# Kernel optimization log

Hardware: AMD Instinct MI355X
Metric: run time of the kernel (lower is better)

Reference implementation:

```python
import jax, jax.numpy as jnp
import numpy as np

B, S, HID = 2, 1024, 2048
N_HEADS, N_KV, HEAD_DIM = 32, 4, 128
BLOCK, MAX_BLOCKS = 32, 128
EPS = 1e-6
ROPE_THETA = 1e6


def _rmsnorm(x, w):
    # per-head RMSNorm over head_dim (Qwen3MoeRMSNorm)
    var = jnp.mean(x * x, axis=-1, keepdims=True)
    return x * jax.lax.rsqrt(var + EPS) * w


def _rotate_half(x):
    h = x.shape[-1] // 2
    return jnp.concatenate([-x[..., h:], x[..., :h]], axis=-1)


def setup_inputs() -> dict:
    key = jax.random.key(0)
    ks = jax.random.split(key, 8)
    hidden_states = jax.random.normal(ks[0], (B, S, HID), dtype=jnp.float32)
    wq = jax.random.normal(ks[1], (N_HEADS * HEAD_DIM, HID), dtype=jnp.float32) * 0.02
    wk = jax.random.normal(ks[2], (N_KV * HEAD_DIM, HID), dtype=jnp.float32) * 0.02
    wv = jax.random.normal(ks[3], (N_KV * HEAD_DIM, HID), dtype=jnp.float32) * 0.02
    wo = jax.random.normal(ks[4], (HID, N_HEADS * HEAD_DIM), dtype=jnp.float32) * 0.02
    q_norm_w = 1.0 + 0.01 * jax.random.normal(ks[5], (HEAD_DIM,), dtype=jnp.float32)
    k_norm_w = 1.0 + 0.01 * jax.random.normal(ks[6], (HEAD_DIM,), dtype=jnp.float32)
    # RoPE tables (rotate-half / llama convention)
    inv_freq = 1.0 / (ROPE_THETA ** (jnp.arange(0, HEAD_DIM, 2, dtype=jnp.float32) / HEAD_DIM))
    t = jnp.arange(S, dtype=jnp.float32)
    freqs = jnp.outer(t, inv_freq)  # [S, HEAD_DIM/2]
    emb = jnp.concatenate([freqs, freqs], axis=-1)  # [S, HEAD_DIM]
    cos, sin = jnp.cos(emb), jnp.sin(emb)
    # page table: B sequences x (S/BLOCK) blocks, distinct block ids
    page_table = jnp.arange(B * (S // BLOCK), dtype=jnp.int32).reshape(B, S // BLOCK)
    return {"hidden_states": hidden_states, "wq": wq, "wk": wk, "wv": wv, "wo": wo,
            "q_norm_w": q_norm_w, "k_norm_w": k_norm_w, "cos": cos, "sin": sin,
            "page_table": page_table}


def reference(hidden_states, wq, wk, wv, wo, q_norm_w, k_norm_w, cos, sin, page_table):
    b, s, _ = hidden_states.shape
    # fused QKV projection (math-equivalent to the concatenated qkv_proj_weight)
    q = (hidden_states @ wq.T).reshape(b, s, N_HEADS, HEAD_DIM)
    k = (hidden_states @ wk.T).reshape(b, s, N_KV, HEAD_DIM)
    v = (hidden_states @ wv.T).reshape(b, s, N_KV, HEAD_DIM)
    # per-head RMSNorm then RoPE
    q = _rmsnorm(q, q_norm_w)
    k = _rmsnorm(k, k_norm_w)
    c = cos[None, :, None, :]
    sn = sin[None, :, None, :]
    q = q * c + _rotate_half(q) * sn
    k = k * c + _rotate_half(k) * sn
    # paged KV-cache fill: [B, nblk, BLOCK, kvh, hd] -> cache[block_id, kvh, BLOCK, hd]
    nblk = s // BLOCK
    k_blk = k.reshape(b, nblk, BLOCK, N_KV, HEAD_DIM).transpose(0, 1, 3, 2, 4).reshape(-1, N_KV, BLOCK, HEAD_DIM)
    v_blk = v.reshape(b, nblk, BLOCK, N_KV, HEAD_DIM).transpose(0, 1, 3, 2, 4).reshape(-1, N_KV, BLOCK, HEAD_DIM)
    flat_pt = page_table.reshape(-1)
    cache_k = jnp.zeros((MAX_BLOCKS, N_KV, BLOCK, HEAD_DIM), dtype=k.dtype).at[flat_pt].set(k_blk)
    cache_v = jnp.zeros((MAX_BLOCKS, N_KV, BLOCK, HEAD_DIM), dtype=v.dtype).at[flat_pt].set(v_blk)
    # GQA: repeat kv heads (num_key_value_groups = 8)
    groups = N_HEADS // N_KV
    k_rep = jnp.repeat(k, groups, axis=2)  # [b, s, N_HEADS, hd]
    v_rep = jnp.repeat(v, groups, axis=2)
    # causal SDPA, scaling = head_dim ** -0.5
    scale = HEAD_DIM ** -0.5
    scores = jnp.einsum('bqhd,bkhd->bhqk', q, k_rep) * scale
    causal = jnp.tril(jnp.ones((s, s), dtype=bool))
    scores = jnp.where(causal[None, None], scores, jnp.finfo(scores.dtype).min)
    probs = jax.nn.softmax(scores, axis=-1)
    attn = jnp.einsum('bhqk,bkhd->bqhd', probs, v_rep).reshape(b, s, N_HEADS * HEAD_DIM)
    out = attn @ wo.T  # [b, s, HID]
    return out, cache_k, cache_v
```

## Files before the change

### kernel.cpp

```cpp
#include <hip/hip_runtime.h>
#include <hip/hip_bf16.h>


typedef __attribute__((ext_vector_type(8))) __bf16 bf16x8;
typedef __attribute__((ext_vector_type(4))) __bf16 bf16x4;
typedef __attribute__((ext_vector_type(4))) float f32x4;

__device__ __forceinline__ void gload16(const void* g, void* l) {
    __builtin_amdgcn_global_load_lds((const __attribute__((address_space(1))) void*)g,
                                     (__attribute__((address_space(3))) void*)l, 16, 0, 0);
}

__global__ __launch_bounds__(256) void cvt5(const float* __restrict__ s0, const float* __restrict__ s1,
                                            const float* __restrict__ s2, const float* __restrict__ s3,
                                            const float* __restrict__ s4,
                                            __bf16* __restrict__ d0, __bf16* __restrict__ d1,
                                            __bf16* __restrict__ d2, __bf16* __restrict__ d3,
                                            __bf16* __restrict__ d4) {
    const int b = blockIdx.x;
    const float* src; __bf16* dst; int off;
    if (b < 4096)       { src = s0; dst = d0; off = b; }
    else if (b < 12288) { src = s1; dst = d1; off = b - 4096; }
    else if (b < 13312) { src = s2; dst = d2; off = b - 12288; }
    else if (b < 14336) { src = s3; dst = d3; off = b - 13312; }
    else                { src = s4; dst = d4; off = b - 14336; }
    const int i = off * 256 + threadIdx.x;
    float4 v = reinterpret_cast<const float4*>(src)[i];
    bf16x4 o = {(__bf16)v.x, (__bf16)v.y, (__bf16)v.z, (__bf16)v.w};
    reinterpret_cast<bf16x4*>(dst)[i] = o;
}

__global__ __launch_bounds__(256) void reduce_add(float* __restrict__ o,
                                                  const float* __restrict__ p, int n4) {
    int i = blockIdx.x * 256 + threadIdx.x;
    int stride = gridDim.x * 256;
    for (; i < n4; i += stride) {
        float4 a = reinterpret_cast<float4*>(o)[i];
        float4 b = reinterpret_cast<const float4*>(p)[i];
        a.x += b.x; a.y += b.y; a.z += b.z; a.w += b.w;
        reinterpret_cast<float4*>(o)[i] = a;
    }
}

template <int NF, int OUT_BF16>
__global__ __launch_bounds__(512, 2) void gemm8p(const __bf16* __restrict__ A,
                                                 const __bf16* __restrict__ B,
                                                 void* __restrict__ C0,
                                                 void* __restrict__ C1,
                                                 const int M, const int N, const int K,
                                                 const int nTiles, const int nbn,
                                                 const int klen) {
    __shared__ __bf16 Asm[2 * 128 * 64];
    __shared__ __bf16 Bsm[2 * NF * 64 * 64];
    const int tid = threadIdx.x, lane = tid & 63, wave = tid >> 6;
    const int wm = wave >> 2, wn = wave & 3;
    const int lrow = lane & 15, lkg = lane >> 4;
    const int rsw = lrow & 7;
    const int bid = blockIdx.x;
    const int kz = bid / nTiles, tile = bid % nTiles;
    const int tswz = (tile & 7) * (nTiles >> 3) + (tile >> 3);
    const int bm = tswz / nbn, bn = tswz % nbn;
    const int brow = bm * 128, bcol = bn * (NF * 64);
    const int kbeg = kz * klen;
    const int row0 = tid >> 3;
    const int scol_sw = ((tid & 7) ^ (row0 & 7)) * 8;
    const __bf16* gA = A + (size_t)(brow + row0) * K + kbeg + scol_sw;
    const __bf16* gB = B + (size_t)(bcol + row0) * K + kbeg + scol_sw;
    const int slot0 = (lkg ^ rsw) * 8;
    const int slot1 = ((4 + lkg) ^ rsw) * 8;
    const int nt = klen / 64, nIter = nt / 2;

    f32x4 acc[4][NF] = {};
    bf16x8 areg[2], breg[NF];

    int su_t = 0, su_w = 0;
    auto stage1 = [&]() {
        if (su_t < nt) {
            const size_t ko = (size_t)su_t * 64;
            if (su_w < 2)
                gload16(gA + (size_t)(su_w * 64) * K + ko,
                        Asm + (su_t & 1) * 8192 + su_w * 4096 + tid * 8);
            else
                gload16(gB + (size_t)((su_w - 2) * 64) * K + ko,
                        Bsm + (su_t & 1) * (NF * 4096) + (su_w - 2) * 4096 + tid * 8);
        }
        if (++su_w == NF + 2) { su_w = 0; ++su_t; }
    };

    for (int u = 0; u < NF + 4; ++u) stage1();
    asm volatile("s_waitcnt vmcnt(2)" ::: "memory");
    __builtin_amdgcn_s_barrier();

    for (int i = 0; i < nIter; ++i) {
        const bool last = (i == nIter - 1);
#pragma unroll
        for (int p = 0; p < 8; ++p) {
            const int q = p & 3, kk = q >> 1, mfh = q & 1, cbuf = p >> 2;
            const __bf16* As = Asm + cbuf * 8192;
            const __bf16* Bs = Bsm + cbuf * (NF * 4096);
            const int ks = kk ? slot1 : slot0;
            if (mfh == 0) {
#pragma unroll
                for (int nf = 0; nf < NF; ++nf)
                    breg[nf] = *reinterpret_cast<const bf16x8*>(
                        &Bs[(wn * (NF * 16) + nf * 16 + lrow) * 64 + ks]);
            }
#pragma unroll
            for (int mi = 0; mi < 2; ++mi)
                areg[mi] = *reinterpret_cast<const bf16x8*>(
                    &As[(wm * 64 + (mfh * 2 + mi) * 16 + lrow) * 64 + ks]);
            const int cp = (NF == 5) ? ((q == 2) ? 1 : 2)
                                     : ((q == 1 || q == 2) ? 1 : 2);
            stage1();
            if (cp == 2) stage1();
            if (p == 3) {
                if (last) asm volatile("s_waitcnt vmcnt(0)" ::: "memory");
                else      asm volatile("s_waitcnt vmcnt(2)" ::: "memory");
            } else if (p == 7 && !last) {
                asm volatile("s_waitcnt vmcnt(2)" ::: "memory");
            }
            __builtin_amdgcn_s_barrier();
            asm volatile("s_waitcnt lgkmcnt(0)" ::: "memory");
            __builtin_amdgcn_sched_barrier(0);
            __builtin_amdgcn_s_setprio(1);
#pragma unroll
            for (int mi = 0; mi < 2; ++mi)
#pragma unroll
                for (int nf = 0; nf < NF; ++nf)
                    acc[mfh * 2 + mi][nf] = __builtin_amdgcn_mfma_f32_16x16x32_bf16(
                        areg[mi], breg[nf], acc[mfh * 2 + mi][nf], 0, 0, 0);
            __builtin_amdgcn_s_setprio(0);
            __builtin_amdgcn_s_barrier();
        }
    }

    void* C = (kz == 0) ? C0 : C1;
#pragma unroll
    for (int mi = 0; mi < 4; ++mi)
#pragma unroll
        for (int nf = 0; nf < NF; ++nf)
#pragma unroll
            for (int j = 0; j < 4; ++j) {
                const size_t r = brow + wm * 64 + mi * 16 + lkg * 4 + j;
                const size_t c = bcol + wn * (NF * 16) + nf * 16 + lrow;
                if (OUT_BF16)
                    ((__bf16*)C)[r * N + c] = (__bf16)acc[mi][nf][j];
                else
                    ((float*)C)[r * N + c] = acc[mi][nf][j];
            }
}

__global__ __launch_bounds__(256) void norm_rope_cache(
    __bf16* __restrict__ qkv, const float* __restrict__ cosT, const float* __restrict__ sinT,
    const float* __restrict__ qw, const float* __restrict__ kw,
    const int* __restrict__ ptab, float* __restrict__ cacheK, float* __restrict__ cacheV) {
    const int t = blockIdx.x;
    const int b = t >> 10, s = t & 1023;
    const int wave = threadIdx.x >> 6, lane = threadIdx.x & 63;
    __bf16* row = qkv + (size_t)t * 5120;
    const float c = cosT[s * 128 + lane];
    const float sn = sinT[s * 128 + lane];
    const int page = ptab[b * 32 + (s >> 5)];
    const int so = s & 31;
    const float wq0 = qw[lane], wq1 = qw[lane + 64];
#pragma unroll
    for (int i = 0; i < 8; ++i) {
        const int h = wave * 8 + i;
        float x0 = (float)row[h * 128 + lane];
        float x1 = (float)row[h * 128 + 64 + lane];
        float ss = x0 * x0 + x1 * x1;
        for (int off = 32; off; off >>= 1) ss += __shfl_xor(ss, off);
        const float rs = rsqrtf(ss * (1.0f / 128.0f) + 1e-6f);
        const float y0 = x0 * rs * wq0, y1 = x1 * rs * wq1;
        row[h * 128 + lane]      = (__bf16)(y0 * c - y1 * sn);
        row[h * 128 + 64 + lane] = (__bf16)(y1 * c + y0 * sn);
    }
    {
        const int h = wave;
        float x0 = (float)row[4096 + h * 128 + lane];
        float x1 = (float)row[4096 + h * 128 + 64 + lane];
        float ss = x0 * x0 + x1 * x1;
        for (int off = 32; off; off >>= 1) ss += __shfl_xor(ss, off);
        const float rs = rsqrtf(ss * (1.0f / 128.0f) + 1e-6f);
        const float y0 = x0 * rs * kw[lane], y1 = x1 * rs * kw[lane + 64];
        const float o0 = y0 * c - y1 * sn, o1 = y1 * c + y0 * sn;
        row[4096 + h * 128 + lane]      = (__bf16)o0;
        row[4096 + h * 128 + 64 + lane] = (__bf16)o1;
        float* ck = cacheK + (((size_t)page * 4 + h) * 32 + so) * 128;
        ck[lane] = o0; ck[lane + 64] = o1;
        const float v0 = (float)row[4608 + h * 128 + lane];
        const float v1 = (float)row[4608 + h * 128 + 64 + lane];
        float* cv = cacheV + (((size_t)page * 4 + h) * 32 + so) * 128;
        cv[lane] = v0; cv[lane + 64] = v1;
    }
}

__global__ __launch_bounds__(512, 2) void attn_fwd(const __bf16* __restrict__ qkv,
                                                   __bf16* __restrict__ out) {
    __shared__ __bf16 Ks[2][64 * 128];
    __shared__ __bf16 Vs[2][128 * 64];
    __shared__ __bf16 Ps[8][2][16 * 64];
    const int qa = blockIdx.x;
    const int qbig = 63 - qa;
    const int kvg = blockIdx.y, b = blockIdx.z;
    const int tid = threadIdx.x, wave = tid >> 6, lane = tid & 63;
    const int lrow = lane & 15, lkg = lane >> 4;
    const int h = kvg * 8 + wave;
    const size_t base = (size_t)b * 1024 * 5120;
    const int kofs = 4096 + kvg * 128, vofs = 4608 + kvg * 128;
    const int ntA = qa / 4 + 1, nt = qbig / 4 + 1;
    const int qposA = qa * 16 + lrow, qposB = qbig * 16 + lrow;
    const int rsw = lrow & 7;

    bf16x8 aqA[4], aqB[4];
#pragma unroll
    for (int kc = 0; kc < 4; ++kc) {
        bf16x8 ta = *reinterpret_cast<const bf16x8*>(
            &qkv[base + (size_t)(qa * 16 + lrow) * 5120 + h * 128 + kc * 32 + lkg * 8]);
        bf16x8 tb = *reinterpret_cast<const bf16x8*>(
            &qkv[base + (size_t)(qbig * 16 + lrow) * 5120 + h * 128 + kc * 32 + lkg * 8]);
#pragma unroll
        for (int i = 0; i < 8; ++i) {
            ta[i] = (__bf16)((float)ta[i] * 0.08838834764831845f);
            tb[i] = (__bf16)((float)tb[i] * 0.08838834764831845f);
        }
        aqA[kc] = ta; aqB[kc] = tb;
    }

    f32x4 accA[8] = {}, accB[8] = {};
    float mA = -1e30f, lA = 0.f, mB = -1e30f, lB = 0.f;
    __bf16* PwA = &Ps[wave][0][0];
    __bf16* PwB = &Ps[wave][1][0];

    auto stageK = [&](int t, int buf) {
        const int kv0 = (t < nt) ? t * 64 : 0;
#pragma unroll
        for (int c = 0; c < 2; ++c) {
            const int chunk = c * 8 + wave;
            const int row = chunk * 4 + (lane >> 4);
            const int gslot = (lane & 15) ^ (row & 7);
            gload16(&qkv[base + (size_t)(kv0 + row) * 5120 + kofs + gslot * 8],
                    &Ks[buf][chunk * 512]);
        }
    };
    auto loadV = [&](int t, uint4 (&vr)[2]) {
        const int kv0 = (t < nt) ? t * 64 : 0;
#pragma unroll
        for (int r = 0; r < 2; ++r)
            vr[r] = *reinterpret_cast<const uint4*>(
                &qkv[base + (size_t)(kv0 + lane) * 5120 + vofs + wave * 16 + r * 8]);
    };
    auto writeV = [&](uint4 (&vr)[2], int buf) {
#pragma unroll
        for (int r = 0; r < 2; ++r) {
            const __bf16* pv = reinterpret_cast<const __bf16*>(&vr[r]);
#pragma unroll
            for (int j = 0; j < 8; ++j) {
                const int d = wave * 16 + r * 8 + j;
                Vs[buf][d * 64 + (((lane >> 3) ^ j) << 3) + (lane & 7)] = pv[j];
            }
        }
    };

    auto smax = [&](f32x4 (&st)[4], float& m_i, float& l_i, f32x4 (&acc)[8],
                    int qpos, int kv0, bool maskit, __bf16* Pw) {
        float sv[16]; float pmax = -1e30f;
#pragma unroll
        for (int f = 0; f < 4; ++f)
#pragma unroll
            for (int j = 0; j < 4; ++j) {
                float x = st[f][j];
                if (maskit) {
                    const int kvpos = kv0 + f * 16 + lkg * 4 + j;
                    if (kvpos > qpos) x = -1e30f;
                }
                sv[f * 4 + j] = x;
                pmax = fmaxf(pmax, x);
            }
        pmax = fmaxf(pmax, __shfl_xor(pmax, 16));
        pmax = fmaxf(pmax, __shfl_xor(pmax, 32));
        if (!__all(pmax - m_i <= 8.f)) {
            const float m_new = fmaxf(m_i, pmax);
            const float sf = __expf(m_i - m_new);
            m_i = m_new;
            l_i *= sf;
            float sfj[4];
#pragma unroll
            for (int j = 0; j < 4; ++j) sfj[j] = __shfl(sf, lkg * 4 + j);
#pragma unroll
            for (int f = 0; f < 8; ++f)
#pragma unroll
                for (int j = 0; j < 4; ++j) acc[f][j] *= sfj[j];
        }
        float ladd = 0.f;
#pragma unroll
        for (int f = 0; f < 4; ++f) {
            bf16x4 pb;
#pragma unroll
            for (int j = 0; j < 4; ++j) {
                const float p = __expf(sv[f * 4 + j] - m_i);
                ladd += p;
                pb[j] = (__bf16)p;
            }
            const int slot = (f * 2 + (lkg >> 1)) ^ rsw;
            *reinterpret_cast<bf16x4*>(&Pw[lrow * 64 + slot * 8 + (lkg & 1) * 4]) = pb;
        }
        ladd += __shfl_xor(ladd, 16);
        ladd += __shfl_xor(ladd, 32);
        l_i += ladd;
    };

    auto body = [&](int t, uint4 (&vcur)[2], uint4 (&vnext)[2]) {
        const int kbuf = t & 1;
        __builtin_amdgcn_s_barrier();
        asm volatile("" ::: "memory");
        loadV(t + 1, vnext);
        stageK(t + 1, kbuf ^ 1);
        asm volatile("s_waitcnt vmcnt(4)" ::: "memory");
        writeV(vcur, kbuf);
        asm volatile("s_waitcnt lgkmcnt(0)" ::: "memory");
        __builtin_amdgcn_s_barrier();
        asm volatile("" ::: "memory");

        const bool doA = t < ntA;
        f32x4 stA[4] = {}, stB[4] = {};
#pragma unroll
        for (int kc = 0; kc < 4; ++kc)
#pragma unroll
            for (int f = 0; f < 4; ++f) {
                bf16x8 ak = *reinterpret_cast<const bf16x8*>(
                    &Ks[kbuf][(f * 16 + lrow) * 128 + (((kc * 4 + lkg) ^ rsw) << 3)]);
                stB[f] = __builtin_amdgcn_mfma_f32_16x16x32_bf16(ak, aqB[kc], stB[f], 0, 0, 0);
                if (doA)
                    stA[f] = __builtin_amdgcn_mfma_f32_16x16x32_bf16(ak, aqA[kc], stA[f], 0, 0, 0);
            }
        if (doA) smax(stA, mA, lA, accA, qposA, t * 64, t == ntA - 1, PwA);
        smax(stB, mB, lB, accB, qposB, t * 64, t == nt - 1, PwB);
#pragma unroll
        for (int kk = 0; kk < 2; ++kk) {
            const int pslot = ((kk * 4 + lkg) ^ rsw) << 3;
            bf16x8 apB = *reinterpret_cast<const bf16x8*>(&PwB[lrow * 64 + pslot]);
            bf16x8 apA;
            if (doA) apA = *reinterpret_cast<const bf16x8*>(&PwA[lrow * 64 + pslot]);
#pragma unroll
            for (int f = 0; f < 8; ++f) {
                bf16x8 bv = *reinterpret_cast<const bf16x8*>(
                    &Vs[kbuf][(f * 16 + lrow) * 64 + pslot]);
                accB[f] = __builtin_amdgcn_mfma_f32_16x16x32_bf16(apB, bv, accB[f], 0, 0, 0);
                if (doA)
                    accA[f] = __builtin_amdgcn_mfma_f32_16x16x32_bf16(apA, bv, accA[f], 0, 0, 0);
            }
        }
    };

    uint4 vrA[2], vrB[2];
    loadV(0, vrA);
    stageK(0, 0);
    for (int t = 0; t < nt; t += 2) {
        body(t, vrA, vrB);
        if (t + 1 < nt) body(t + 1, vrB, vrA);
    }
    asm volatile("s_waitcnt vmcnt(0)" ::: "memory");

    float linvA[4], linvB[4];
#pragma unroll
    for (int j = 0; j < 4; ++j) {
        linvA[j] = 1.0f / __shfl(lA, lkg * 4 + j);
        linvB[j] = 1.0f / __shfl(lB, lkg * 4 + j);
    }
#pragma unroll
    for (int f = 0; f < 8; ++f)
#pragma unroll
        for (int j = 0; j < 4; ++j) {
            out[((size_t)b * 1024 + qa * 16 + lkg * 4 + j) * 4096 + h * 128 + f * 16 + lrow] =
                (__bf16)(accA[f][j] * linvA[j]);
            out[((size_t)b * 1024 + qbig * 16 + lkg * 4 + j) * 4096 + h * 128 + f * 16 + lrow] =
                (__bf16)(accB[f][j] * linvB[j]);
        }
}

extern "C" void kernel_launch(void* const* d_in, const int* in_sizes, int n_in,
                              void* d_out, int out_size, void* d_ws, size_t ws_size,
                              hipStream_t stream) {
    const float* hidden = (const float*)d_in[0];
    const float* wq = (const float*)d_in[1];
    const float* wk = (const float*)d_in[2];
    const float* wv = (const float*)d_in[3];
    const float* wo = (const float*)d_in[4];
    const float* qnw = (const float*)d_in[5];
    const float* knw = (const float*)d_in[6];
    const float* cosT = (const float*)d_in[7];
    const float* sinT = (const float*)d_in[8];
    const int* ptab = (const int*)d_in[9];

    float* outp = (float*)d_out;
    float* cacheK = outp + 4194304;
    float* cacheV = cacheK + 2097152;

    char* ws = (char*)d_ws;
    __bf16* hbf    = (__bf16*)ws;
    __bf16* w1bf   = (__bf16*)(ws + 8388608);
    __bf16* wobf   = (__bf16*)(ws + 29360128);
    __bf16* qkvbf  = (__bf16*)(ws + 46137344);
    __bf16* attnbf = (__bf16*)ws;
    float*  opart  = (float*)(ws + 46137344);

    cvt5<<<22528, 256, 0, stream>>>(hidden, wq, wk, wv, wo,
                                    hbf, w1bf, w1bf + (size_t)4096 * 2048,
                                    w1bf + (size_t)4608 * 2048, wobf);

    gemm8p<5, 1><<<256, 512, 0, stream>>>(hbf, w1bf, qkvbf, nullptr,
                                          2048, 5120, 2048, 256, 16, 2048);

    hipMemsetAsync(cacheK, 0, (size_t)4194304 * 4, stream);
    norm_rope_cache<<<2048, 256, 0, stream>>>(qkvbf, cosT, sinT, qnw, knw, ptab, cacheK, cacheV);

    attn_fwd<<<dim3(32, 4, 2), 512, 0, stream>>>(qkvbf, attnbf);

    gemm8p<4, 0><<<256, 512, 0, stream>>>(attnbf, wobf, outp, opart,
                                          2048, 2048, 4096, 128, 8, 2048);
    reduce_add<<<2048, 256, 0, stream>>>(outp, opart, 4194304 / 4);
}
```

Before: 201.7 us.

## Restructure GEMM pipeline to 4-phase per tile and split attention blocks by head halves

The GEMM main loop drops the 8-phase interleaved schedule, which had fine-grained load staging and a barrier per phase. In its place each K tile gets two half-K MFMA phases, and the next tile's global-to-LDS loads are all issued at once mid-tile, leaving fewer barriers per tile. Attention goes from 512-thread blocks covering 8 heads of a KV group to 256-thread blocks covering 4 heads, which doubles the grid. This is meant to improve occupancy and load balance, at the cost of each block reloading the shared K/V tiles. The larger per-thread V load raises vmcnt thresholds, and fewer barriers in the GEMM may expose load latency.

```diff
diff --git a/kernel.cpp b/kernel.cpp
--- a/kernel.cpp
+++ b/kernel.cpp
@@ -43,7 +43,7 @@
 }
 
 template <int NF, int OUT_BF16>
-__global__ __launch_bounds__(512, 2) void gemm8p(const __bf16* __restrict__ A,
+__global__ __launch_bounds__(512, 2) void gemm4p(const __bf16* __restrict__ A,
                                                  const __bf16* __restrict__ B,
                                                  void* __restrict__ C0,
                                                  void* __restrict__ C1,
@@ -68,10 +68,10 @@
     const __bf16* gB = B + (size_t)(bcol + row0) * K + kbeg + scol_sw;
     const int slot0 = (lkg ^ rsw) * 8;
     const int slot1 = ((4 + lkg) ^ rsw) * 8;
-    const int nt = klen / 64, nIter = nt / 2;
+    const int nt = klen / 64;
+    constexpr int UPT = NF + 2;
 
     f32x4 acc[4][NF] = {};
-    bf16x8 areg[2], breg[NF];
 
     int su_t = 0, su_w = 0;
     auto stage1 = [&]() {
@@ -84,54 +84,58 @@
                 gload16(gB + (size_t)((su_w - 2) * 64) * K + ko,
                         Bsm + (su_t & 1) * (NF * 4096) + (su_w - 2) * 4096 + tid * 8);
         }
-        if (++su_w == NF + 2) { su_w = 0; ++su_t; }
-    };
-
-    for (int u = 0; u < NF + 4; ++u) stage1();
-    asm volatile("s_waitcnt vmcnt(2)" ::: "memory");
+        if (++su_w == UPT) { su_w = 0; ++su_t; }
+    };
+
+    for (int u = 0; u < 2 * UPT; ++u) stage1();
+    if constexpr (NF == 5) asm volatile("s_waitcnt vmcnt(7)" ::: "memory");
+    else                   asm volatile("s_waitcnt vmcnt(6)" ::: "memory");
     __builtin_amdgcn_s_barrier();
 
-    for (int i = 0; i < nIter; ++i) {
-        const bool last = (i == nIter - 1);
-#pragma unroll
-        for (int p = 0; p < 8; ++p) {
-            const int q = p & 3, kk = q >> 1, mfh = q & 1, cbuf = p >> 2;
-            const __bf16* As = Asm + cbuf * 8192;
-            const __bf16* Bs = Bsm + cbuf * (NF * 4096);
-            const int ks = kk ? slot1 : slot0;
-            if (mfh == 0) {
-#pragma unroll
-                for (int nf = 0; nf < NF; ++nf)
-                    breg[nf] = *reinterpret_cast<const bf16x8*>(
-                        &Bs[(wn * (NF * 16) + nf * 16 + lrow) * 64 + ks]);
-            }
-#pragma unroll
-            for (int mi = 0; mi < 2; ++mi)
-                areg[mi] = *reinterpret_cast<const bf16x8*>(
-                    &As[(wm * 64 + (mfh * 2 + mi) * 16 + lrow) * 64 + ks]);
-            const int cp = (NF == 5) ? ((q == 2) ? 1 : 2)
-                                     : ((q == 1 || q == 2) ? 1 : 2);
-            stage1();
-            if (cp == 2) stage1();
-            if (p == 3) {
-                if (last) asm volatile("s_waitcnt vmcnt(0)" ::: "memory");
-                else      asm volatile("s_waitcnt vmcnt(2)" ::: "memory");
-            } else if (p == 7 && !last) {
-                asm volatile("s_waitcnt vmcnt(2)" ::: "memory");
-            }
-            __builtin_amdgcn_s_barrier();
-            asm volatile("s_waitcnt lgkmcnt(0)" ::: "memory");
-            __builtin_amdgcn_sched_barrier(0);
-            __builtin_amdgcn_s_setprio(1);
-#pragma unroll
-            for (int mi = 0; mi < 2; ++mi)
-#pragma unroll
-                for (int nf = 0; nf < NF; ++nf)
-                    acc[mfh * 2 + mi][nf] = __builtin_amdgcn_mfma_f32_16x16x32_bf16(
-                        areg[mi], breg[nf], acc[mfh * 2 + mi][nf], 0, 0, 0);
-            __builtin_amdgcn_s_setprio(0);
-            __builtin_amdgcn_s_barrier();
-        }
+    for (int t = 0; t < nt; ++t) {
+        const __bf16* As = Asm + (t & 1) * 8192;
+        const __bf16* Bs = Bsm + (t & 1) * (NF * 4096);
+        bf16x8 ar[4], br[NF];
+#pragma unroll
+        for (int mi = 0; mi < 4; ++mi)
+            ar[mi] = *reinterpret_cast<const bf16x8*>(&As[(wm * 64 + mi * 16 + lrow) * 64 + slot0]);
+#pragma unroll
+        for (int nf = 0; nf < NF; ++nf)
+            br[nf] = *reinterpret_cast<const bf16x8*>(&Bs[(wn * (NF * 16) + nf * 16 + lrow) * 64 + slot0]);
+        asm volatile("s_waitcnt lgkmcnt(0)" ::: "memory");
+        __builtin_amdgcn_sched_barrier(0);
+        __builtin_amdgcn_s_setprio(1);
+#pragma unroll
+        for (int mi = 0; mi < 4; ++mi)
+#pragma unroll
+            for (int nf = 0; nf < NF; ++nf)
+                acc[mi][nf] = __builtin_amdgcn_mfma_f32_16x16x32_bf16(ar[mi], br[nf], acc[mi][nf], 0, 0, 0);
+        __builtin_amdgcn_s_setprio(0);
+        __builtin_amdgcn_s_barrier();
+#pragma unroll
+        for (int mi = 0; mi < 4; ++mi)
+            ar[mi] = *reinterpret_cast<const bf16x8*>(&As[(wm * 64 + mi * 16 + lrow) * 64 + slot1]);
+#pragma unroll
+        for (int nf = 0; nf < NF; ++nf)
+            br[nf] = *reinterpret_cast<const bf16x8*>(&Bs[(wn * (NF * 16) + nf * 16 + lrow) * 64 + slot1]);
+        asm volatile("s_waitcnt lgkmcnt(0)" ::: "memory");
+#pragma unroll
+        for (int u = 0; u < UPT; ++u) stage1();
+        __builtin_amdgcn_sched_barrier(0);
+        __builtin_amdgcn_s_setprio(1);
+#pragma unroll
+        for (int mi = 0; mi < 4; ++mi)
+#pragma unroll
+            for (int nf = 0; nf < NF; ++nf)
+                acc[mi][nf] = __builtin_amdgcn_mfma_f32_16x16x32_bf16(ar[mi], br[nf], acc[mi][nf], 0, 0, 0);
+        __builtin_amdgcn_s_setprio(0);
+        if (t + 2 < nt) {
+            if constexpr (NF == 5) asm volatile("s_waitcnt vmcnt(7)" ::: "memory");
+            else                   asm volatile("s_waitcnt vmcnt(6)" ::: "memory");
+        } else {
+            asm volatile("s_waitcnt vmcnt(0)" ::: "memory");
+        }
+        __builtin_amdgcn_s_barrier();
     }
 
     void* C = (kz == 0) ? C0 : C1;
@@ -195,17 +199,19 @@
     }
 }
 
-__global__ __launch_bounds__(512, 2) void attn_fwd(const __bf16* __restrict__ qkv,
+__global__ __launch_bounds__(256, 2) void attn_fwd(const __bf16* __restrict__ qkv,
                                                    __bf16* __restrict__ out) {
     __shared__ __bf16 Ks[2][64 * 128];
     __shared__ __bf16 Vs[2][128 * 64];
-    __shared__ __bf16 Ps[8][2][16 * 64];
+    __shared__ __bf16 Ps[4][16 * 64];
     const int qa = blockIdx.x;
     const int qbig = 63 - qa;
-    const int kvg = blockIdx.y, b = blockIdx.z;
+    const int yy = blockIdx.y;
+    const int kvg = yy >> 1, hh = yy & 1;
+    const int b = blockIdx.z;
     const int tid = threadIdx.x, wave = tid >> 6, lane = tid & 63;
     const int lrow = lane & 15, lkg = lane >> 4;
-    const int h = kvg * 8 + wave;
+    const int h = kvg * 8 + hh * 4 + wave;
     const size_t base = (size_t)b * 1024 * 5120;
     const int kofs = 4096 + kvg * 128, vofs = 4608 + kvg * 128;
     const int ntA = qa / 4 + 1, nt = qbig / 4 + 1;
@@ -229,41 +235,40 @@
 
     f32x4 accA[8] = {}, accB[8] = {};
     float mA = -1e30f, lA = 0.f, mB = -1e30f, lB = 0.f;
-    __bf16* PwA = &Ps[wave][0][0];
-    __bf16* PwB = &Ps[wave][1][0];
+    __bf16* Pw = &Ps[wave][0];
 
     auto stageK = [&](int t, int buf) {
         const int kv0 = (t < nt) ? t * 64 : 0;
 #pragma unroll
-        for (int c = 0; c < 2; ++c) {
-            const int chunk = c * 8 + wave;
+        for (int c = 0; c < 4; ++c) {
+            const int chunk = c * 4 + wave;
             const int row = chunk * 4 + (lane >> 4);
             const int gslot = (lane & 15) ^ (row & 7);
             gload16(&qkv[base + (size_t)(kv0 + row) * 5120 + kofs + gslot * 8],
                     &Ks[buf][chunk * 512]);
         }
     };
-    auto loadV = [&](int t, uint4 (&vr)[2]) {
+    auto loadV = [&](int t, uint4 (&vr)[4]) {
         const int kv0 = (t < nt) ? t * 64 : 0;
 #pragma unroll
-        for (int r = 0; r < 2; ++r)
+        for (int r = 0; r < 4; ++r)
             vr[r] = *reinterpret_cast<const uint4*>(
-                &qkv[base + (size_t)(kv0 + lane) * 5120 + vofs + wave * 16 + r * 8]);
-    };
-    auto writeV = [&](uint4 (&vr)[2], int buf) {
-#pragma unroll
-        for (int r = 0; r < 2; ++r) {
+                &qkv[base + (size_t)(kv0 + lane) * 5120 + vofs + wave * 32 + r * 8]);
+    };
+    auto writeV = [&](uint4 (&vr)[4], int buf) {
+#pragma unroll
+        for (int r = 0; r < 4; ++r) {
             const __bf16* pv = reinterpret_cast<const __bf16*>(&vr[r]);
 #pragma unroll
             for (int j = 0; j < 8; ++j) {
-                const int d = wave * 16 + r * 8 + j;
+                const int d = wave * 32 + r * 8 + j;
                 Vs[buf][d * 64 + (((lane >> 3) ^ j) << 3) + (lane & 7)] = pv[j];
             }
         }
     };
 
     auto smax = [&](f32x4 (&st)[4], float& m_i, float& l_i, f32x4 (&acc)[8],
-                    int qpos, int kv0, bool maskit, __bf16* Pw) {
+                    int qpos, int kv0, bool maskit) {
         float sv[16]; float pmax = -1e30f;
 #pragma unroll
         for (int f = 0; f < 4; ++f)
@@ -310,13 +315,27 @@
         l_i += ladd;
     };
 
-    auto body = [&](int t, uint4 (&vcur)[2], uint4 (&vnext)[2]) {
+    auto pv = [&](f32x4 (&acc)[8], int kbuf) {
+#pragma unroll
+        for (int kk = 0; kk < 2; ++kk) {
+            const int pslot = ((kk * 4 + lkg) ^ rsw) << 3;
+            bf16x8 ap = *reinterpret_cast<const bf16x8*>(&Pw[lrow * 64 + pslot]);
+#pragma unroll
+            for (int f = 0; f < 8; ++f) {
+                bf16x8 bv = *reinterpret_cast<const bf16x8*>(
+                    &Vs[kbuf][(f * 16 + lrow) * 64 + pslot]);
+                acc[f] = __builtin_amdgcn_mfma_f32_16x16x32_bf16(ap, bv, acc[f], 0, 0, 0);
+            }
+        }
+    };
+
+    auto body = [&](int t, uint4 (&vcur)[4], uint4 (&vnext)[4]) {
         const int kbuf = t & 1;
         __builtin_amdgcn_s_barrier();
         asm volatile("" ::: "memory");
         loadV(t + 1, vnext);
         stageK(t + 1, kbuf ^ 1);
-        asm volatile("s_waitcnt vmcnt(4)" ::: "memory");
+        asm volatile("s_waitcnt vmcnt(8)" ::: "memory");
         writeV(vcur, kbuf);
         asm volatile("s_waitcnt lgkmcnt(0)" ::: "memory");
         __builtin_amdgcn_s_barrier();
@@ -334,26 +353,15 @@
                 if (doA)
                     stA[f] = __builtin_amdgcn_mfma_f32_16x16x32_bf16(ak, aqA[kc], stA[f], 0, 0, 0);
             }
-        if (doA) smax(stA, mA, lA, accA, qposA, t * 64, t == ntA - 1, PwA);
-        smax(stB, mB, lB, accB, qposB, t * 64, t == nt - 1, PwB);
-#pragma unroll
-        for (int kk = 0; kk < 2; ++kk) {
-            const int pslot = ((kk * 4 + lkg) ^ rsw) << 3;
-            bf16x8 apB = *reinterpret_cast<const bf16x8*>(&PwB[lrow * 64 + pslot]);
-            bf16x8 apA;
-            if (doA) apA = *reinterpret_cast<const bf16x8*>(&PwA[lrow * 64 + pslot]);
-#pragma unroll
-            for (int f = 0; f < 8; ++f) {
-                bf16x8 bv = *reinterpret_cast<const bf16x8*>(
-                    &Vs[kbuf][(f * 16 + lrow) * 64 + pslot]);
-                accB[f] = __builtin_amdgcn_mfma_f32_16x16x32_bf16(apB, bv, accB[f], 0, 0, 0);
-                if (doA)
-                    accA[f] = __builtin_amdgcn_mfma_f32_16x16x32_bf16(apA, bv, accA[f], 0, 0, 0);
-            }
-        }
-    };
-
-    uint4 vrA[2], vrB[2];
+        if (doA) {
+            smax(stA, mA, lA, accA, qposA, t * 64, t == ntA - 1);
+            pv(accA, kbuf);
+        }
+        smax(stB, mB, lB, accB, qposB, t * 64, t == nt - 1);
+        pv(accB, kbuf);
+    };
+
+    uint4 vrA[4], vrB[4];
     loadV(0, vrA);
     stageK(0, 0);
     for (int t = 0; t < nt; t += 2) {
@@ -409,15 +417,15 @@
                                     hbf, w1bf, w1bf + (size_t)4096 * 2048,
                                     w1bf + (size_t)4608 * 2048, wobf);
 
-    gemm8p<5, 1><<<256, 512, 0, stream>>>(hbf, w1bf, qkvbf, nullptr,
+    gemm4p<5, 1><<<256, 512, 0, stream>>>(hbf, w1bf, qkvbf, nullptr,
                                           2048, 5120, 2048, 256, 16, 2048);
 
     hipMemsetAsync(cacheK, 0, (size_t)4194304 * 4, stream);
     norm_rope_cache<<<2048, 256, 0, stream>>>(qkvbf, cosT, sinT, qnw, knw, ptab, cacheK, cacheV);
 
-    attn_fwd<<<dim3(32, 4, 2), 512, 0, stream>>>(qkvbf, attnbf);
-
-    gemm8p<4, 0><<<256, 512, 0, stream>>>(attnbf, wobf, outp, opart,
+    attn_fwd<<<dim3(32, 8, 2), 256, 0, stream>>>(qkvbf, attnbf);
+
+    gemm4p<4, 0><<<256, 512, 0, stream>>>(attnbf, wobf, outp, opart,
                                           2048, 2048, 4096, 128, 8, 2048);
     reduce_add<<<2048, 256, 0, stream>>>(outp, opart, 4194304 / 4);
 }
```

Measured after the change: 213.0 us. 5.6% more time.
